# Performance work log

Hardware: AMD Instinct MI355X
Metric: run time of the kernel (lower is better)

The kernel has to match this reference:

```python
import jax, jax.numpy as jnp
import numpy as np

N = 20000      # num_sr == num_tg entities
D = 256        # ent_dim
DR = 256       # rel_dim
RNUM = 1000    # number of relations
Q = 128        # SVD rank
H = 4          # n_head
L = 2          # layers
E_RAND = 640000  # random edges (avg degree 32); N self-loops appended
LEAK = 0.2
EPS_LN = 1e-5


def _l2norm(x):
    # F.normalize(x, dim=1, p=2)
    return x / jnp.maximum(jnp.linalg.norm(x, axis=1, keepdims=True), 1e-12)


def _gat(x, src, dst, W, a_s, a_d):
    """Multi-head GAT layer on an edge list; heads are averaged so out dim == in dim.
    x: [N,D], W: [H,D,D], a_s/a_d: [H,D]."""
    n = x.shape[0]
    h = jnp.einsum('nd,hde->nhe', x, W)                  # [N,H,D]
    es = jnp.einsum('nhe,he->nh', h, a_s)                # [N,H]
    ed = jnp.einsum('nhe,he->nh', h, a_d)                # [N,H]
    e = jax.nn.leaky_relu(es[src] + ed[dst], LEAK)       # [E,H]
    # segment softmax over incoming edges of each dst node
    m = jax.ops.segment_max(e, dst, num_segments=n)      # [N,H]
    ex = jnp.exp(e - m[dst])
    den = jax.ops.segment_sum(ex, dst, num_segments=n)   # [N,H]
    attn = ex / (den[dst] + 1e-16)                       # [E,H]
    out = jax.ops.segment_sum(attn[:, :, None] * h[src], dst, num_segments=n)  # [N,H,D]
    return jax.nn.elu(out).mean(axis=1)                  # head average -> [N,D]


def _mha(x, wq, bq, wk, bk, wv, bv, fc_w, fc_b, ln_g, ln_b):
    """Standard post-norm multi-head self-attention over the 'ranges' axis. x: [N,R,D]."""
    n, r, d = x.shape
    def split(y):  # [N,R,H*D] -> [N,H,R,D]
        return y.reshape(n, r, H, d).transpose(0, 2, 1, 3)
    q, k, v = split(x @ wq + bq), split(x @ wk + bk), split(x @ wv + bv)
    attn = jax.nn.softmax(jnp.einsum('nhqd,nhkd->nhqk', q, k) / jnp.sqrt(jnp.float32(d)), axis=-1)
    o = jnp.einsum('nhqk,nhkd->nhqd', attn, v).transpose(0, 2, 1, 3).reshape(n, r, H * d)
    o = o @ fc_w + fc_b + x                              # output proj + residual
    mu = o.mean(-1, keepdims=True)
    var = o.var(-1, keepdims=True)
    return (o - mu) / jnp.sqrt(var + EPS_LN) * ln_g + ln_b


def _rel_agg(adj_in, adj_out, rel):
    # sparse-dense mm + row-sum normalize + concat (direct=True branch)
    ri = (adj_in @ rel) / (adj_in.sum(-1, keepdims=True) + 1e-5)
    ro = (adj_out @ rel) / (adj_out.sum(-1, keepdims=True) + 1e-5)
    return jnp.concatenate([ri, ro], axis=-1)            # [N, 2*DR]


def _forward(ent_sr, ent_tg, rel_sr, rel_tg, alpha,
             u_mul_s_sr, vt_sr, u_mul_s_tg, vt_tg,
             rel_adj_sr_in, rel_adj_sr_out, rel_adj_tg_in, rel_adj_tg_out,
             gat_W, gat_a_src, gat_a_dst,
             wq, bq, wk, bk, wv, bv, fc_w, fc_b, ln_g, ln_b,
             edges_sr, edges_tg):
    # --- Relation Aggregator (direct=True, phase='eval': aug == aggregated) ---
    sr_rel = _rel_agg(rel_adj_sr_in, rel_adj_sr_out, rel_sr)
    tg_rel = _rel_agg(rel_adj_tg_in, rel_adj_tg_out, rel_tg)
    aug_sr_rel, aug_tg_rel = sr_rel, tg_rel

    # --- Global Structure Aggregator: SVD-based propagation ---
    e_sr, e_tg = ent_sr, ent_tg
    for _ in range(L):
        g_sr = u_mul_s_sr @ (vt_sr @ e_sr)               # [N,Q]@([Q,N]@[N,D])
        g_tg = u_mul_s_tg @ (vt_tg @ e_tg)
        e_sr = jax.nn.relu(alpha * g_sr + (1.0 - alpha) * e_sr)
        e_tg = jax.nn.relu(alpha * g_tg + (1.0 - alpha) * e_tg)
    aug_sr = e_sr + ent_sr
    aug_tg = e_tg + ent_tg

    # --- Attentive Neighbor Aggregator (res=True; eval => dropout = identity) ---
    x_sr, x_tg = ent_sr, ent_tg
    sr_list, tg_list = [x_sr], [x_tg]
    for l in range(L):
        x_sr = _l2norm(_gat(x_sr, edges_sr[0], edges_sr[1], gat_W[l], gat_a_src[l], gat_a_dst[l]))
        x_tg = _l2norm(_gat(x_tg, edges_tg[0], edges_tg[1], gat_W[l], gat_a_src[l], gat_a_dst[l]))
        sr_list.append(x_sr)
        tg_list.append(x_tg)

    # --- multi-range neighborhood fusion ---
    sr = _mha(jnp.stack(sr_list, axis=1), wq, bq, wk, bk, wv, bv, fc_w, fc_b, ln_g, ln_b).mean(axis=1)
    tg = _mha(jnp.stack(tg_list, axis=1), wq, bq, wk, bk, wv, bv, fc_w, fc_b, ln_g, ln_b).mean(axis=1)

    # --- final fusion: neighbors + relation semantics ---
    sr_out = jnp.concatenate([sr, sr_rel], axis=-1)
    tg_out = jnp.concatenate([tg, tg_rel], axis=-1)
    aug_sr_out = jnp.concatenate([aug_sr, aug_sr_rel], axis=-1)
    aug_tg_out = jnp.concatenate([aug_tg, aug_tg_rel], axis=-1)
    return (sr_out, tg_out, aug_sr_out, aug_tg_out)


def setup_inputs() -> dict:
    key = jax.random.key(0)
    ks = jax.random.split(key, 32)
    def nrm(k, shape, s):
        return jax.random.normal(k, shape, jnp.float32) * s
    def edges(k):
        e = jax.random.randint(k, (2, E_RAND), 0, N, dtype=jnp.int32)
        loops = jnp.arange(N, dtype=jnp.int32)
        return jnp.concatenate([e, jnp.stack([loops, loops])], axis=1)  # [2, E_RAND+N]
    inp = {
        'ent_sr': nrm(ks[0], (N, D), 0.1),
        'ent_tg': nrm(ks[1], (N, D), 0.1),
        'rel_sr': nrm(ks[2], (RNUM, DR), 0.1),
        'rel_tg': nrm(ks[3], (RNUM, DR), 0.1),
        'alpha': jnp.float32(0.5),
        'u_mul_s_sr': nrm(ks[4], (N, Q), 0.05),
        'vt_sr': nrm(ks[5], (Q, N), 0.05),
        'u_mul_s_tg': nrm(ks[6], (N, Q), 0.05),
        'vt_tg': nrm(ks[7], (Q, N), 0.05),
        'rel_adj_sr_in': jax.random.uniform(ks[8], (N, RNUM), jnp.float32),
        'rel_adj_sr_out': jax.random.uniform(ks[9], (N, RNUM), jnp.float32),
        'rel_adj_tg_in': jax.random.uniform(ks[10], (N, RNUM), jnp.float32),
        'rel_adj_tg_out': jax.random.uniform(ks[11], (N, RNUM), jnp.float32),
        'gat_W': nrm(ks[12], (L, H, D, D), 1.0 / np.sqrt(D)),
        'gat_a_src': nrm(ks[13], (L, H, D), 1.0 / np.sqrt(D)),
        'gat_a_dst': nrm(ks[14], (L, H, D), 1.0 / np.sqrt(D)),
        'wq': nrm(ks[15], (D, H * D), 1.0 / np.sqrt(D)),
        'bq': jnp.zeros((H * D,), jnp.float32),
        'wk': nrm(ks[16], (D, H * D), 1.0 / np.sqrt(D)),
        'bk': jnp.zeros((H * D,), jnp.float32),
        'wv': nrm(ks[17], (D, H * D), 1.0 / np.sqrt(D)),
        'bv': jnp.zeros((H * D,), jnp.float32),
        'fc_w': nrm(ks[18], (H * D, D), 1.0 / np.sqrt(H * D)),
        'fc_b': jnp.zeros((D,), jnp.float32),
        'ln_g': jnp.ones((D,), jnp.float32),
        'ln_b': jnp.zeros((D,), jnp.float32),
        'edges_sr': edges(ks[19]),
        'edges_tg': edges(ks[20]),
    }
    return inp


def reference(ent_sr, ent_tg, rel_sr, rel_tg, alpha,
              u_mul_s_sr, vt_sr, u_mul_s_tg, vt_tg,
              rel_adj_sr_in, rel_adj_sr_out, rel_adj_tg_in, rel_adj_tg_out,
              gat_W, gat_a_src, gat_a_dst,
              wq, bq, wk, bk, wv, bv, fc_w, fc_b, ln_g, ln_b,
              edges_sr, edges_tg):
    return _forward(ent_sr, ent_tg, rel_sr, rel_tg, alpha,
                    u_mul_s_sr, vt_sr, u_mul_s_tg, vt_tg,
                    rel_adj_sr_in, rel_adj_sr_out, rel_adj_tg_in, rel_adj_tg_out,
                    gat_W, gat_a_src, gat_a_dst,
                    wq, bq, wk, bk, wv, bv, fc_w, fc_b, ln_g, ln_b,
                    edges_sr, edges_tg)
```

## Files before the change

### kernel.cpp

```cpp
#include <hip/hip_runtime.h>
#include <stdint.h>

typedef unsigned short u16;
typedef __bf16 bf16x8 __attribute__((ext_vector_type(8)));
typedef float f32x4 __attribute__((ext_vector_type(4)));

#define DEV static __device__ __forceinline__

DEV float bf2f(u16 u) { unsigned v = ((unsigned)u) << 16; float f; __builtin_memcpy(&f, &v, 4); return f; }
DEV u16 f2bf(float f) {
  unsigned x; __builtin_memcpy(&x, &f, 4);
  x += 0x7FFFu + ((x >> 16) & 1u);
  return (u16)(x >> 16);
}
DEV float wred_sum(float v) { for (int m = 32; m; m >>= 1) v += __shfl_xor(v, m); return v; }
DEV float wred_max(float v) { for (int m = 32; m; m >>= 1) v = fmaxf(v, __shfl_xor(v, m)); return v; }
DEV void wred_max4(f32x4& v) {
  for (int m = 32; m; m >>= 1) {
#pragma unroll
    for (int i = 0; i < 4; ++i) v[i] = fmaxf(v[i], __shfl_xor(v[i], m));
  }
}
DEV void wred_sum4(f32x4& v) {
  for (int m = 32; m; m >>= 1) {
#pragma unroll
    for (int i = 0; i < 4; ++i) v[i] += __shfl_xor(v[i], m);
  }
}

enum { M_ATOMIC = 0, M_SCALE2, M_BLEND, M_BF16, M_BF16B, M_F32B, M_PART };

template <int MODE>
__global__ __launch_bounds__(256) void k_gemm(
    const u16* __restrict__ A, const u16* __restrict__ B,
    int M, int lda, int ldb, int Ksteps, int kper,
    void* __restrict__ C1v, float* __restrict__ C2, int ldc,
    const float* __restrict__ rowsum, const float* __restrict__ ein, int ldein,
    const float* __restrict__ alphap, const float* __restrict__ bias,
    long hA, long hB, long hC, int nsplit, long hE)
{
  __shared__ u16 As[4096], Bs[4096];
  const int tid = threadIdx.x, lane = tid & 63, wid = tid >> 6;
  const long m0 = (long)blockIdx.x * 128, n0 = (long)blockIdx.y * 128;
  int ks, kend;
  long chead = 0;
  int hz = 0;
  if (hA | hB | hC) {
    int z = blockIdx.z;
    hz = z / nsplit;
    int sp = z - hz * nsplit;
    A += (long)hz * hA;
    B += (long)hz * hB;
    chead = (MODE == M_PART) ? (long)z * hC : (long)hz * hC;
    ks = sp * kper;
    kend = ks + kper; if (kend > Ksteps) kend = Ksteps;
  } else {
    ks = blockIdx.z * kper;
    kend = ks + kper; if (kend > Ksteps) kend = Ksteps;
  }
  if (MODE == M_BLEND) ein += (long)hz * hE;

  const u16 *ag[2], *bg[2];
  u16 *al[2], *bl[2];
#pragma unroll
  for (int i = 0; i < 2; ++i) {
    int s = (wid * 2 + i) * 64 + lane;
    int row = s >> 2, cs = (s & 3) ^ ((row >> 1) & 3);
    ag[i] = A + (m0 + row) * (long)lda + cs * 8;
    bg[i] = B + (n0 + row) * (long)ldb + cs * 8;
    al[i] = As + (wid * 2 + i) * 512;
    bl[i] = Bs + (wid * 2 + i) * 512;
  }
  const int kq = lane >> 4, rr = lane & 15;
  const int wm = wid >> 1, wn = wid & 1;

  f32x4 acc[4][4] = {};

  for (; ks < kend; ++ks) {
    long ko = (long)ks * 32;
#pragma unroll
    for (int i = 0; i < 2; ++i) {
      __builtin_amdgcn_global_load_lds((const __attribute__((address_space(1))) unsigned int*)(ag[i] + ko),
                                       (__attribute__((address_space(3))) unsigned int*)al[i], 16, 0, 0);
      __builtin_amdgcn_global_load_lds((const __attribute__((address_space(1))) unsigned int*)(bg[i] + ko),
                                       (__attribute__((address_space(3))) unsigned int*)bl[i], 16, 0, 0);
    }
    __syncthreads();
    bf16x8 af[4], bff[4];
#pragma unroll
    for (int i = 0; i < 4; ++i) {
      int ra = wm * 64 + i * 16 + rr, ca = kq ^ ((ra >> 1) & 3);
      af[i] = *(const bf16x8*)(As + ra * 32 + ca * 8);
      int rb = wn * 64 + i * 16 + rr, cb = kq ^ ((rb >> 1) & 3);
      bff[i] = *(const bf16x8*)(Bs + rb * 32 + cb * 8);
    }
#pragma unroll
    for (int i = 0; i < 4; ++i)
#pragma unroll
      for (int j = 0; j < 4; ++j)
        acc[i][j] = __builtin_amdgcn_mfma_f32_16x16x32_bf16(af[i], bff[j], acc[i][j], 0, 0, 0);
    __syncthreads();
  }

  float* Cf = (float*)C1v;
  u16* Cu = (u16*)C1v;
  const int r4 = (lane >> 4) << 2;
#pragma unroll
  for (int i = 0; i < 4; ++i) {
#pragma unroll
    for (int rg = 0; rg < 4; ++rg) {
      long row = m0 + wm * 64 + i * 16 + r4 + rg;
      if (row >= M) continue;
      float scale = 0.f, al_ = 0.f, ml_ = 0.f;
      if (MODE == M_SCALE2) scale = 1.f / (rowsum[(long)hz * M + row] + 1e-5f);
      if (MODE == M_BLEND) { al_ = *alphap; ml_ = 1.f - al_; }
#pragma unroll
      for (int j = 0; j < 4; ++j) {
        long col = n0 + wn * 64 + j * 16 + rr;
        float v = acc[i][j][rg];
        long idx = chead + row * (long)ldc + col;
        if (MODE == M_ATOMIC) atomicAdd(Cf + idx, v);
        else if (MODE == M_PART) Cf[idx] = v;
        else if (MODE == M_SCALE2) { float sv = v * scale; Cf[idx] = sv; C2[idx] = sv; }
        else if (MODE == M_BLEND) { float e = ein[row * (long)ldein + col]; Cf[idx] = fmaxf(al_ * v + ml_ * e, 0.f); }
        else if (MODE == M_BF16) Cu[idx] = f2bf(v);
        else if (MODE == M_BF16B) Cu[idx] = f2bf(v + bias[col]);
        else if (MODE == M_F32B) Cf[idx] = v + bias[col];
      }
    }
  }
}

__global__ void k_cvt(const float* __restrict__ in, u16* __restrict__ out, long R, long C, long Cp, long ostride)
{
  long idx = (long)blockIdx.x * blockDim.x + threadIdx.x;
  long cw = Cp >> 3;
  if (idx >= R * cw) return;
  long r = idx / cw, c8 = (idx % cw) << 3;
  u16 tmp[8];
  if (c8 < C) {
    const f32x4* p = (const f32x4*)(in + r * C + c8);
    f32x4 a = p[0], b = p[1];
#pragma unroll
    for (int i = 0; i < 4; ++i) { tmp[i] = f2bf(a[i]); tmp[4 + i] = f2bf(b[i]); }
  } else {
#pragma unroll
    for (int i = 0; i < 8; ++i) tmp[i] = 0;
  }
  uint4 w_; __builtin_memcpy(&w_, tmp, 16);
  *(uint4*)(out + r * ostride + c8) = w_;
}

__global__ __launch_bounds__(256) void k_cvtT(const float* __restrict__ in, u16* __restrict__ out,
                                              int Bh, int R, int C, int Rp)
{
  __shared__ float tile[64][65];
  int bid = blockIdx.x;
  int nrt = Rp >> 6;
  int rt = bid % nrt; bid /= nrt;
  int nct = C >> 6;
  int ct = bid % nct; int b = bid / nct;
  int t = threadIdx.x;
  int tr = t >> 4, tc4 = (t & 15) << 2;
#pragma unroll
  for (int i = 0; i < 4; ++i) {
    int r = (rt << 6) + tr + i * 16;
    f32x4 v = {0.f, 0.f, 0.f, 0.f};
    if (r < R) v = *(const f32x4*)(in + ((long)b * R + r) * C + (ct << 6) + tc4);
    tile[tr + i * 16][tc4 + 0] = v[0];
    tile[tr + i * 16][tc4 + 1] = v[1];
    tile[tr + i * 16][tc4 + 2] = v[2];
    tile[tr + i * 16][tc4 + 3] = v[3];
  }
  __syncthreads();
  int wc = t >> 4, wr4 = (t & 15) << 2;
#pragma unroll
  for (int i = 0; i < 4; ++i) {
    int c = wc + i * 16;
    u16 o[4];
#pragma unroll
    for (int k2 = 0; k2 < 4; ++k2) o[k2] = f2bf(tile[wr4 + k2][c]);
    unsigned long long pk; __builtin_memcpy(&pk, o, 8);
    *(unsigned long long*)(out + ((long)b * C + (ct << 6) + c) * Rp + (rt << 6) + wr4) = pk;
  }
}

__global__ __launch_bounds__(256) void k_adj4(const float* __restrict__ a0, const float* __restrict__ a1,
                                              const float* __restrict__ a2, const float* __restrict__ a3,
                                              u16* __restrict__ o01, u16* __restrict__ o23,
                                              float* __restrict__ rowsum, int C, int Cp, int N)
{
  int r = blockIdx.x, pl = blockIdx.y, t = threadIdx.x;
  const float* in = pl == 0 ? a0 : pl == 1 ? a1 : pl == 2 ? a2 : a3;
  u16* out = pl < 2 ? o01 + (size_t)pl * N * Cp : o23 + (size_t)(pl - 2) * N * Cp;
  f32x4 v = {0.f, 0.f, 0.f, 0.f};
  int c = t << 2;
  if (c + 3 < C) v = *(const f32x4*)(in + (long)r * C + c);
  u16 o[4];
#pragma unroll
  for (int i = 0; i < 4; ++i) o[i] = f2bf(v[i]);
  unsigned long long pk; __builtin_memcpy(&pk, o, 8);
  *(unsigned long long*)(out + (long)r * Cp + c) = pk;
  float s = wred_sum(v[0] + v[1] + v[2] + v[3]);
  __shared__ float ws4[4];
  if ((t & 63) == 0) ws4[t >> 6] = s;
  __syncthreads();
  if (t == 0) rowsum[(long)pl * N + r] = ws4[0] + ws4[1] + ws4[2] + ws4[3];
}

__global__ void k_red(const float* __restrict__ P, float* __restrict__ o, int NS)
{
  int i = blockIdx.x * 256 + threadIdx.x;
  int h = i >> 15, rem = i & 32767;
  const float* p = P + (long)h * NS * 32768 + rem;
  float s = 0.f;
  for (int k = 0; k < NS; ++k) s += p[(long)k * 32768];
  o[i] = s;
}

__global__ void k_zero_i(int* p, int n) { for (int i = blockIdx.x * blockDim.x + threadIdx.x; i < n; i += gridDim.x * blockDim.x) p[i] = 0; }
__global__ void k_copy_i(const int* __restrict__ a, int* __restrict__ b, int n) { for (int i = blockIdx.x * blockDim.x + threadIdx.x; i < n; i += gridDim.x * blockDim.x) b[i] = a[i]; }
__global__ void k_hist(const int* __restrict__ dst, int* __restrict__ deg, int E)
{ for (int i = blockIdx.x * blockDim.x + threadIdx.x; i < E; i += gridDim.x * blockDim.x) atomicAdd(&deg[dst[i]], 1); }
__global__ void k_scatter(const int* __restrict__ src, const int* __restrict__ dst, int* __restrict__ cur,
                          int* __restrict__ srcs, int E)
{
  for (int i = blockIdx.x * blockDim.x + threadIdx.x; i < E; i += gridDim.x * blockDim.x) {
    int p = atomicAdd(&cur[dst[i]], 1);
    srcs[p] = src[i];
  }
}
__global__ __launch_bounds__(1024) void k_scan(const int* __restrict__ deg, int* __restrict__ off, int n)
{
  __shared__ int bsum[1024];
  int t = threadIdx.x;
  int per = (n + 1023) >> 10;
  int s0 = t * per, s1 = s0 + per; if (s1 > n) s1 = n;
  int s = 0;
  for (int i = s0; i < s1; ++i) s += deg[i];
  bsum[t] = s;
  __syncthreads();
  for (int d = 1; d < 1024; d <<= 1) {
    int x = (t >= d) ? bsum[t - d] : 0;
    __syncthreads();
    bsum[t] += x;
    __syncthreads();
  }
  if (t == 0) off[0] = 0;
  int run = t ? bsum[t - 1] : 0;
  for (int i = s0; i < s1; ++i) { run += deg[i]; off[i + 1] = run; }
}

__global__ __launch_bounds__(256) void k_esed(const u16* __restrict__ h, const float* __restrict__ as_,
                                              const float* __restrict__ ad_, float* __restrict__ esq,
                                              float* __restrict__ ed, signed char* __restrict__ q8, int N)
{
  int n = blockIdx.x, t = threadIdx.x, hd = t >> 6, l = t & 63;
  long base = (long)n * 1024 + hd * 256 + (l << 2);
  ushort4 hv = *(const ushort4*)(h + base);
  float h0 = bf2f(hv.x), h1 = bf2f(hv.y), h2 = bf2f(hv.z), h3 = bf2f(hv.w);
  const float* ap = as_ + hd * 256 + (l << 2);
  const float* dp = ad_ + hd * 256 + (l << 2);
  float ps = h0 * ap[0] + h1 * ap[1] + h2 * ap[2] + h3 * ap[3];
  float pd = h0 * dp[0] + h1 * dp[1] + h2 * dp[2] + h3 * dp[3];
  ps = wred_sum(ps); pd = wred_sum(pd);
  float amax = fmaxf(fmaxf(fabsf(h0), fabsf(h1)), fmaxf(fabsf(h2), fabsf(h3)));
  amax = wred_max(amax);
  float rsc = amax > 0.f ? 127.f / amax : 0.f;
  signed char qb[4];
  qb[0] = (signed char)__float2int_rn(h0 * rsc);
  qb[1] = (signed char)__float2int_rn(h1 * rsc);
  qb[2] = (signed char)__float2int_rn(h2 * rsc);
  qb[3] = (signed char)__float2int_rn(h3 * rsc);
  int qw; __builtin_memcpy(&qw, qb, 4);
  *(int*)(q8 + base) = qw;
  if (l == 0) {
    esq[n * 8 + hd] = ps;
    esq[n * 8 + 4 + hd] = amax * (1.f / 127.f);
    ed[n * 4 + hd] = pd;
  }
}

__global__ __launch_bounds__(256) void k_gat(const signed char* __restrict__ q8,
                                             const float* __restrict__ esq, const float* __restrict__ ed,
                                             const int* __restrict__ off0, const int* __restrict__ srcs0,
                                             const int* __restrict__ off1, const int* __restrict__ srcs1,
                                             u16* __restrict__ x0, u16* __restrict__ x1, int N, int NPq)
{
  int t = threadIdx.x, w = t >> 6, l = t & 63;
  int n = blockIdx.x * 4 + w;
  if (n >= N) return;
  int side = blockIdx.y;
  const int* off = side ? off1 : off0;
  const int* srcs = side ? srcs1 : srcs0;
  u16* xout = side ? x1 : x0;
  size_t ofs = side ? (size_t)NPq : 0;
  q8 += ofs * 1024; esq += ofs * 8;

  int e0 = off[n], deg = off[n + 1] - e0;
  f32x4 edv = *(const f32x4*)(ed + (ofs + n) * 4);

  f32x4 m = {-1e30f, -1e30f, -1e30f, -1e30f};
  f32x4 psum = {0.f, 0.f, 0.f, 0.f};
  f32x4 acc0 = {0.f, 0.f, 0.f, 0.f};
  f32x4 acc1 = {0.f, 0.f, 0.f, 0.f};
  f32x4 acc2 = {0.f, 0.f, 0.f, 0.f};
  f32x4 acc3 = {0.f, 0.f, 0.f, 0.f};
  const long loff = l << 2;

  for (int base = 0; base < deg; base += 64) {
    int cnt = min(64, deg - base);
    bool act = l < cnt;
    int s = 0;
    f32x4 v = {-1e30f, -1e30f, -1e30f, -1e30f};
    if (act) {
      s = srcs[e0 + base + l];
      f32x4 es4 = *(const f32x4*)(esq + (long)s * 8);
#pragma unroll
      for (int hd = 0; hd < 4; ++hd) {
        float x = es4[hd] + edv[hd];
        v[hd] = x >= 0.f ? x : 0.2f * x;
      }
    }
    f32x4 mc = v;
    wred_max4(mc);
    f32x4 nm;
#pragma unroll
    for (int hd = 0; hd < 4; ++hd) nm[hd] = fmaxf(m[hd], mc[hd]);
    f32x4 sc;
#pragma unroll
    for (int hd = 0; hd < 4; ++hd) sc[hd] = __expf(m[hd] - nm[hd]);
    psum *= sc;
    acc0 *= sc[0]; acc1 *= sc[1]; acc2 *= sc[2]; acc3 *= sc[3];
    m = nm;
    f32x4 wq4 = {0.f, 0.f, 0.f, 0.f};
    if (act) {
      f32x4 qs4 = *(const f32x4*)(esq + (long)s * 8 + 4);
#pragma unroll
      for (int hd = 0; hd < 4; ++hd) {
        float e = __expf(v[hd] - m[hd]);
        psum[hd] += e;
        wq4[hd] = e * qs4[hd];
      }
    }
#pragma unroll 2
    for (int j = 0; j < cnt; ++j) {
      int sj = __shfl(s, j);
      float w0 = __shfl(wq4[0], j);
      float w1 = __shfl(wq4[1], j);
      float w2 = __shfl(wq4[2], j);
      float w3 = __shfl(wq4[3], j);
      const signed char* p = q8 + (long)sj * 1024 + loff;
      char4 c0 = *(const char4*)(p);
      char4 c1 = *(const char4*)(p + 256);
      char4 c2 = *(const char4*)(p + 512);
      char4 c3 = *(const char4*)(p + 768);
      acc0[0] += w0 * (float)c0.x; acc0[1] += w0 * (float)c0.y; acc0[2] += w0 * (float)c0.z; acc0[3] += w0 * (float)c0.w;
      acc1[0] += w1 * (float)c1.x; acc1[1] += w1 * (float)c1.y; acc1[2] += w1 * (float)c1.z; acc1[3] += w1 * (float)c1.w;
      acc2[0] += w2 * (float)c2.x; acc2[1] += w2 * (float)c2.y; acc2[2] += w2 * (float)c2.z; acc2[3] += w2 * (float)c2.w;
      acc3[0] += w3 * (float)c3.x; acc3[1] += w3 * (float)c3.y; acc3[2] += w3 * (float)c3.z; acc3[3] += w3 * (float)c3.w;
    }
  }
  wred_sum4(psum);
  f32x4 rd;
#pragma unroll
  for (int hd = 0; hd < 4; ++hd) rd[hd] = 1.f / (psum[hd] + 1e-16f);
  float mean[4]; float nrm = 0.f;
#pragma unroll
  for (int i = 0; i < 4; ++i) {
    float y0 = acc0[i] * rd[0]; y0 = y0 > 0.f ? y0 : __expf(y0) - 1.f;
    float y1 = acc1[i] * rd[1]; y1 = y1 > 0.f ? y1 : __expf(y1) - 1.f;
    float y2 = acc2[i] * rd[2]; y2 = y2 > 0.f ? y2 : __expf(y2) - 1.f;
    float y3 = acc3[i] * rd[3]; y3 = y3 > 0.f ? y3 : __expf(y3) - 1.f;
    float mv = 0.25f * (y0 + y1 + y2 + y3);
    mean[i] = mv; nrm += mv * mv;
  }
  nrm = wred_sum(nrm);
  float scn = 1.f / fmaxf(sqrtf(nrm), 1e-12f);
  u16 o[4];
#pragma unroll
  for (int i = 0; i < 4; ++i) o[i] = f2bf(mean[i] * scn);
  unsigned long long pk; __builtin_memcpy(&pk, o, 8);
  *(unsigned long long*)(xout + (long)n * 768 + loff) = pk;
}

__global__ void k_bias2(const float* __restrict__ wq, const float* __restrict__ wk,
                        const float* __restrict__ fcw,
                        const float* __restrict__ bq, const float* __restrict__ bk,
                        const float* __restrict__ bv,
                        float* __restrict__ vq1, float* __restrict__ vq2,
                        float* __restrict__ beff2, float* __restrict__ s3)
{
  int t = blockIdx.x * 256 + threadIdx.x;
  int h = t >> 8, d = t & 255;
  float a1 = 0.f, a2 = 0.f, a3 = 0.f;
  for (int j = 0; j < 256; ++j) {
    a1 += wk[(long)d * 1024 + h * 256 + j] * bq[h * 256 + j];
    a2 += wq[(long)d * 1024 + h * 256 + j] * bk[h * 256 + j];
    a3 += bv[h * 256 + j] * fcw[(long)(h * 256 + j) * 256 + d];
  }
  vq1[t] = a1; vq2[t] = a2; beff2[t] = a3;
  if (d == 0) {
    float s = 0.f;
    for (int j = 0; j < 256; ++j) s += bq[h * 256 + j] * bk[h * 256 + j];
    s3[h] = s;
  }
}

__global__ __launch_bounds__(256) void k_score2(const u16* __restrict__ x, const u16* __restrict__ kg,
                                                const float* __restrict__ vq1, const float* __restrict__ vq2,
                                                const float* __restrict__ s3, float* __restrict__ attn,
                                                int N, int NPq)
{
  int n = blockIdx.x, side = blockIdx.y, t = threadIdx.x, hd = t >> 6, l = t & 63;
  long rbase = (long)side * 3 * NPq + (long)n * 3;
  int i4 = l << 2;
  f32x4 xr[3], kc[3];
#pragma unroll
  for (int r = 0; r < 3; ++r) {
    ushort4 a = *(const ushort4*)(x + (rbase + r) * 256 + i4);
    xr[r][0] = bf2f(a.x); xr[r][1] = bf2f(a.y); xr[r][2] = bf2f(a.z); xr[r][3] = bf2f(a.w);
    ushort4 b = *(const ushort4*)(kg + (rbase + r) * 1024 + hd * 256 + i4);
    kc[r][0] = bf2f(b.x); kc[r][1] = bf2f(b.y); kc[r][2] = bf2f(b.z); kc[r][3] = bf2f(b.w);
  }
  f32x4 v1 = *(const f32x4*)(vq1 + hd * 256 + i4);
  f32x4 v2 = *(const f32x4*)(vq2 + hd * 256 + i4);
  float red[15];
#pragma unroll
  for (int r = 0; r < 3; ++r)
#pragma unroll
    for (int c = 0; c < 3; ++c) {
      f32x4 p = xr[r] * kc[c];
      red[r * 3 + c] = p[0] + p[1] + p[2] + p[3];
    }
#pragma unroll
  for (int c = 0; c < 3; ++c) {
    f32x4 p1 = xr[c] * v1;
    f32x4 p2 = xr[c] * v2;
    red[9 + c] = p1[0] + p1[1] + p1[2] + p1[3];
    red[12 + c] = p2[0] + p2[1] + p2[2] + p2[3];
  }
#pragma unroll
  for (int i = 0; i < 15; ++i) red[i] = wred_sum(red[i]);
  if (l == 0) {
    float s3h = s3[hd];
    float* out = attn + ((long)side * N + n) * 36 + hd * 9;
#pragma unroll
    for (int r = 0; r < 3; ++r) {
      float v0 = (red[r * 3 + 0] + red[9 + 0] + red[12 + r] + s3h) * 0.0625f;
      float v1_ = (red[r * 3 + 1] + red[9 + 1] + red[12 + r] + s3h) * 0.0625f;
      float v2_ = (red[r * 3 + 2] + red[9 + 2] + red[12 + r] + s3h) * 0.0625f;
      float mm = fmaxf(v0, fmaxf(v1_, v2_));
      float e0 = __expf(v0 - mm), e1 = __expf(v1_ - mm), e2 = __expf(v2_ - mm);
      float rs = 1.f / (e0 + e1 + e2);
      out[r * 3 + 0] = e0 * rs; out[r * 3 + 1] = e1 * rs; out[r * 3 + 2] = e2 * rs;
    }
  }
}

__global__ __launch_bounds__(256) void k_cln(const u16* __restrict__ vf, const float* __restrict__ attn,
                                             const u16* __restrict__ x, const float* __restrict__ fcb,
                                             const float* __restrict__ g, const float* __restrict__ b,
                                             float* __restrict__ out0, float* __restrict__ out1,
                                             int N, int NPq)
{
  int n = blockIdx.x, side = blockIdx.y, t = threadIdx.x, w = t >> 6, l = t & 63;
  long rbase = (long)side * 3 * NPq + (long)n * 3;
  float* out = (side ? out1 : out0) + (long)n * 768;
  __shared__ float aa[36];
  __shared__ float ybuf[3][256];
  if (t < 36) aa[t] = attn[((long)side * N + n) * 36 + t];
  __syncthreads();
  if (w < 3) {
    int d4 = l << 2;
    f32x4 acc = {0.f, 0.f, 0.f, 0.f};
#pragma unroll
    for (int h = 0; h < 4; ++h)
#pragma unroll
      for (int rp = 0; rp < 3; ++rp) {
        float wgt = aa[h * 9 + w * 3 + rp];
        ushort4 vv = *(const ushort4*)(vf + (rbase + rp) * 1024 + h * 256 + d4);
        acc[0] += wgt * bf2f(vv.x); acc[1] += wgt * bf2f(vv.y);
        acc[2] += wgt * bf2f(vv.z); acc[3] += wgt * bf2f(vv.w);
      }
    f32x4 fb = *(const f32x4*)(fcb + d4);
    ushort4 xu = *(const ushort4*)(x + (rbase + w) * 256 + d4);
    acc[0] += fb[0] + bf2f(xu.x); acc[1] += fb[1] + bf2f(xu.y);
    acc[2] += fb[2] + bf2f(xu.z); acc[3] += fb[3] + bf2f(xu.w);
    float s1 = acc[0] + acc[1] + acc[2] + acc[3];
    float s2 = acc[0] * acc[0] + acc[1] * acc[1] + acc[2] * acc[2] + acc[3] * acc[3];
    s1 = wred_sum(s1); s2 = wred_sum(s2);
    float mu = s1 * 0.00390625f;
    float var = s2 * 0.00390625f - mu * mu;
    float rs = rsqrtf(var + 1e-5f);
#pragma unroll
    for (int i = 0; i < 4; ++i) {
      int d = d4 + i;
      ybuf[w][d] = (acc[i] - mu) * rs * g[d] + b[d];
    }
  }
  __syncthreads();
  if (t < 64) {
#pragma unroll
    for (int i = 0; i < 4; ++i) {
      int d = (t << 2) + i;
      out[d] = (ybuf[0][d] + ybuf[1][d] + ybuf[2][d]) * (1.f / 3.f);
    }
  }
}

__global__ void k_aug(const float* __restrict__ e, const float* __restrict__ ent0,
                      const float* __restrict__ ent1, float* __restrict__ out, int N)
{
  long i = (long)blockIdx.x * blockDim.x + threadIdx.x;
  if (i >= (long)N * 128) return;
  int side = i >= (long)N * 64;
  long ii = side ? i - (long)N * 64 : i;
  const float* ent = side ? ent1 : ent0;
  long n = ii >> 6; int d4 = (int)(ii & 63) << 2;
  f32x4 a = *(const f32x4*)(e + ((long)side * N + n) * 256 + d4);
  f32x4 c = *(const f32x4*)(ent + n * 256 + d4);
  *(f32x4*)(out + ((long)side * N + n) * 768 + d4) = a + c;
}

extern "C" void kernel_launch(void* const* d_in, const int* in_sizes, int n_in,
                              void* d_out, int out_size, void* d_ws, size_t ws_size,
                              hipStream_t stream)
{
  (void)n_in; (void)out_size; (void)ws_size;
  const int N = 20000, NP = 20096, RNUM = 1000, RP = 1024;
  const int NT2 = NP + N;
  const int NS = 64;
  const int Es = in_sizes[26] / 2, Et = in_sizes[27] / 2;

  const float* ent_sr = (const float*)d_in[0];
  const float* ent_tg = (const float*)d_in[1];
  const float* rel_in[2] = {(const float*)d_in[2], (const float*)d_in[3]};
  const float* alphap = (const float*)d_in[4];
  const float* ums[2] = {(const float*)d_in[5], (const float*)d_in[7]};
  const float* vt[2]  = {(const float*)d_in[6], (const float*)d_in[8]};
  const float* adj[4] = {(const float*)d_in[9], (const float*)d_in[10], (const float*)d_in[11], (const float*)d_in[12]};
  const float* gat_W  = (const float*)d_in[13];
  const float* gat_as = (const float*)d_in[14];
  const float* gat_ad = (const float*)d_in[15];
  const float* wq = (const float*)d_in[16]; const float* bq = (const float*)d_in[17];
  const float* wk = (const float*)d_in[18]; const float* bk = (const float*)d_in[19];
  const float* wv = (const float*)d_in[20]; const float* bv = (const float*)d_in[21];
  const float* fcw = (const float*)d_in[22]; const float* fcb = (const float*)d_in[23];
  const float* lng = (const float*)d_in[24]; const float* lnb = (const float*)d_in[25];
  const int* edges[2] = {(const int*)d_in[26], (const int*)d_in[27]};
  const int Ecnt[2] = {Es, Et};

  float* out0 = (float*)d_out;
  float* out1 = out0 + (size_t)N * 768;
  float* out2 = out1 + (size_t)N * 768;
  float* out3 = out2 + (size_t)N * 768;

  char* wsp = (char*)d_ws; size_t wo = 0;
  auto alloc = [&](size_t bytes) { void* p = wsp + wo; wo = (wo + bytes + 255) & ~(size_t)255; return p; };

  u16* A_sr = (u16*)alloc((size_t)NP * 768 * 2);
  u16* A_tg = (u16*)alloc((size_t)NP * 768 * 2);
  u16* QBUF = (u16*)alloc((size_t)3 * NT2 * 1024 * 2);
  u16* KBUF = (u16*)alloc((size_t)3 * NT2 * 1024 * 2);
  float* PART = (float*)alloc((size_t)2 * NS * 32768 * 4);
  float* rowsum = (float*)alloc((size_t)4 * N * 4);
  u16* relT[2] = {(u16*)alloc(256 * RP * 2), (u16*)alloc(256 * RP * 2)};
  u16* WtG = (u16*)alloc((size_t)2 * 1024 * 256 * 2);
  u16* fcT = (u16*)alloc(256 * 1024 * 2);
  u16* wqB = (u16*)alloc(256 * 1024 * 2);
  u16* wkB = (u16*)alloc(256 * 1024 * 2);
  u16* wvB = (u16*)alloc(256 * 1024 * 2);
  u16* gT  = (u16*)alloc((size_t)4 * 256 * 256 * 2);
  u16* vfT = (u16*)alloc((size_t)4 * 256 * 256 * 2);
  float* vq1 = (float*)alloc(1024 * 4);
  float* vq2 = (float*)alloc(1024 * 4);
  float* beff2 = (float*)alloc(1024 * 4);
  float* s3b = (float*)alloc(4 * 4);
  float* esqb = (float*)alloc((size_t)NT2 * 8 * 4);
  float* edb = (float*)alloc((size_t)NT2 * 4 * 4);
  float* attn = (float*)alloc((size_t)2 * N * 36 * 4);
  int* off_[2]; int* cur_[2]; int* srcs_[2];
  for (int s = 0; s < 2; ++s) {
    off_[s] = (int*)alloc((size_t)(N + 4) * 4);
    cur_[s] = (int*)alloc((size_t)(N + 4) * 4);
    srcs_[s] = (int*)alloc((size_t)Ecnt[s] * 4);
  }
  float* tT2 = (float*)alloc((size_t)2 * 256 * 128 * 4);
  u16* tTb2 = (u16*)alloc((size_t)2 * 256 * 128 * 2);

  u16* hbuf = QBUF;
  u16* vfbuf = QBUF;
  u16* adjbQ = QBUF;
  u16* adjbK = KBUF;
  float* e_b = (float*)KBUF;
  u16* eT = (u16*)(e_b + (size_t)2 * N * 256);
  u16* vtb0 = eT + (size_t)2 * 256 * NP;
  u16* umb0 = vtb0 + (size_t)2 * 128 * NP;
  signed char* q8buf = (signed char*)KBUF;
  u16* kgbuf = KBUF;

  const float* ent_s[2] = {ent_sr, ent_tg};

  auto cvt = [&](const float* in, u16* out, long R, long C, long Cp, long ostr) {
    long total = R * (Cp >> 3);
    int blocks = (int)((total + 255) / 256);
    k_cvt<<<blocks, 256, 0, stream>>>(in, out, R, C, Cp, ostr);
  };
  auto cvtT = [&](const float* in, u16* out, int Bh, int R, int C, int Rp) {
    int blocks = (Rp >> 6) * (C >> 6) * Bh;
    k_cvtT<<<blocks, 256, 0, stream>>>(in, out, Bh, R, C, Rp);
  };
  auto gemm = [&](int mode, const u16* A, const u16* B, int M, int lda, int ldb, int Kp, int Nt,
                  int zdim, int nsplit,
                  void* C1, float* C2, int ldc, const float* rs, const float* ein, int ldein,
                  const float* alp, const float* bias,
                  long hA = 0, long hB = 0, long hC = 0, long hE = 0) {
    int Ks = Kp >> 5;
    bool hmode = (hA | hB | hC) != 0;
    int kper = hmode ? (Ks + nsplit - 1) / nsplit
                     : (zdim > 1 ? (Ks + zdim - 1) / zdim : Ks);
    dim3 g((M + 127) >> 7, Nt, zdim);
    switch (mode) {
      case M_ATOMIC: k_gemm<M_ATOMIC><<<g, 256, 0, stream>>>(A, B, M, lda, ldb, Ks, kper, C1, C2, ldc, rs, ein, ldein, alp, bias, hA, hB, hC, nsplit, hE); break;
      case M_SCALE2: k_gemm<M_SCALE2><<<g, 256, 0, stream>>>(A, B, M, lda, ldb, Ks, kper, C1, C2, ldc, rs, ein, ldein, alp, bias, hA, hB, hC, nsplit, hE); break;
      case M_BLEND:  k_gemm<M_BLEND><<<g, 256, 0, stream>>>(A, B, M, lda, ldb, Ks, kper, C1, C2, ldc, rs, ein, ldein, alp, bias, hA, hB, hC, nsplit, hE); break;
      case M_BF16:   k_gemm<M_BF16><<<g, 256, 0, stream>>>(A, B, M, lda, ldb, Ks, kper, C1, C2, ldc, rs, ein, ldein, alp, bias, hA, hB, hC, nsplit, hE); break;
      case M_BF16B:  k_gemm<M_BF16B><<<g, 256, 0, stream>>>(A, B, M, lda, ldb, Ks, kper, C1, C2, ldc, rs, ein, ldein, alp, bias, hA, hB, hC, nsplit, hE); break;
      case M_F32B:   k_gemm<M_F32B><<<g, 256, 0, stream>>>(A, B, M, lda, ldb, Ks, kper, C1, C2, ldc, rs, ein, ldein, alp, bias, hA, hB, hC, nsplit, hE); break;
      case M_PART:   k_gemm<M_PART><<<g, 256, 0, stream>>>(A, B, M, lda, ldb, Ks, kper, C1, C2, ldc, rs, ein, ldein, alp, bias, hA, hB, hC, nsplit, hE); break;
    }
  };

  for (int s = 0; s < 2; ++s) {
    k_zero_i<<<80, 256, 0, stream>>>(cur_[s], N);
    k_hist<<<1024, 256, 0, stream>>>(edges[s] + Ecnt[s], cur_[s], Ecnt[s]);
    k_scan<<<1, 1024, 0, stream>>>(cur_[s], off_[s], N);
    k_copy_i<<<80, 256, 0, stream>>>(off_[s], cur_[s], N);
    k_scatter<<<1024, 256, 0, stream>>>(edges[s], edges[s] + Ecnt[s], cur_[s], srcs_[s], Ecnt[s]);
  }

  cvtT(rel_in[0], relT[0], 1, RNUM, 256, RP);
  cvtT(rel_in[1], relT[1], 1, RNUM, 256, RP);
  {
    dim3 ga(N, 4);
    k_adj4<<<ga, 256, 0, stream>>>(adj[0], adj[1], adj[2], adj[3], adjbQ, adjbK, rowsum, RNUM, RP, N);
  }
  gemm(M_SCALE2, adjbQ, relT[0], N, RP, RP, RP, 2, 2, 1,
       out0 + 256, out2 + 256, 768, rowsum, nullptr, 0, nullptr, nullptr,
       (long)N * RP, 0, 256);
  gemm(M_SCALE2, adjbK, relT[1], N, RP, RP, RP, 2, 2, 1,
       out1 + 256, out3 + 256, 768, rowsum + 2 * N, nullptr, 0, nullptr, nullptr,
       (long)N * RP, 0, 256);

  cvt(vt[0], vtb0, 128, N, NP, NP);
  cvt(vt[1], vtb0 + (size_t)128 * NP, 128, N, NP, NP);
  cvt(ums[0], umb0, N, 128, 128, 128);
  cvt(ums[1], umb0 + (size_t)NP * 128, N, 128, 128, 128);
  for (int l = 0; l < 2; ++l) {
    if (l == 0) {
      cvtT(ent_sr, eT, 1, N, 256, NP);
      cvtT(ent_tg, eT + (size_t)256 * NP, 1, N, 256, NP);
    } else {
      cvtT(e_b, eT, 2, N, 256, NP);
    }
    gemm(M_PART, eT, vtb0, 256, NP, NP, NP, 1, 2 * NS, NS,
         PART, nullptr, 128, nullptr, nullptr, 0, nullptr, nullptr,
         (long)256 * NP, (long)128 * NP, 32768);
    k_red<<<256, 256, 0, stream>>>(PART, tT2, NS);
    cvt(tT2, tTb2, 512, 128, 128, 128);
    if (l == 0) {
      for (int s = 0; s < 2; ++s)
        gemm(M_BLEND, umb0 + (size_t)s * NP * 128, tTb2 + (size_t)s * 32768, N, 128, 128, 128, 2, 1, 1,
             e_b + (size_t)s * N * 256, nullptr, 256, nullptr, ent_s[s], 256, alphap, nullptr);
    } else {
      gemm(M_BLEND, umb0, tTb2, N, 128, 128, 128, 2, 2, 1,
           e_b, nullptr, 256, nullptr, e_b, 256, alphap, nullptr,
           (long)NP * 128, 32768, (long)N * 256, (long)N * 256);
    }
  }
  k_aug<<<(int)(((long)N * 128 + 255) / 256), 256, 0, stream>>>(e_b, ent_sr, ent_tg, out2, N);

  cvt(ent_sr, A_sr, N, 256, 256, 768);
  cvt(ent_tg, A_tg, N, 256, 256, 768);
  cvtT(gat_W, WtG, 8, 256, 256, 256);
  for (int l = 0; l < 2; ++l) {
    gemm(M_BF16, A_sr + l * 256, WtG + (size_t)l * 1024 * 256, NT2, 768, 256, 256, 8, 1, 1,
         hbuf, nullptr, 1024, nullptr, nullptr, 0, nullptr, nullptr);
    k_esed<<<NT2, 256, 0, stream>>>(hbuf, gat_as + l * 1024, gat_ad + l * 1024, esqb, edb, q8buf, NT2);
    dim3 gg((N + 3) / 4, 2);
    k_gat<<<gg, 256, 0, stream>>>(q8buf, esqb, edb, off_[0], srcs_[0], off_[1], srcs_[1],
                                  A_sr + (l + 1) * 256, A_tg + (l + 1) * 256, N, NP);
  }

  cvt(wq, wqB, 256, 1024, 1024, 1024);
  cvt(wk, wkB, 256, 1024, 1024, 1024);
  cvt(wv, wvB, 256, 1024, 1024, 1024);
  cvtT(fcw, fcT, 1, 1024, 256, 1024);
  k_bias2<<<4, 256, 0, stream>>>(wq, wk, fcw, bq, bk, bv, vq1, vq2, beff2, s3b);
  gemm(M_BF16, wqB, wkB, 256, 1024, 1024, 256, 2, 4, 1, gT, nullptr, 256,
       nullptr, nullptr, 0, nullptr, nullptr, 256, 256, 65536);
  gemm(M_BF16, fcT, wvB, 256, 1024, 1024, 256, 2, 4, 1, vfT, nullptr, 256,
       nullptr, nullptr, 0, nullptr, nullptr, 256, 256, 65536);

  gemm(M_BF16, A_sr, gT, 3 * NT2, 256, 256, 256, 8, 1, 1, kgbuf, nullptr, 1024,
       nullptr, nullptr, 0, nullptr, nullptr);
  {
    dim3 gs(N, 2);
    k_score2<<<gs, 256, 0, stream>>>(A_sr, kgbuf, vq1, vq2, s3b, attn, N, NP);
  }
  gemm(M_BF16B, A_sr, vfT, 3 * NT2, 256, 256, 256, 8, 1, 1, vfbuf, nullptr, 1024,
       nullptr, nullptr, 0, nullptr, beff2);
  {
    dim3 gc(N, 2);
    k_cln<<<gc, 256, 0, stream>>>(vfbuf, attn, A_sr, fcb, lng, lnb, out0, out1, N, NP);
  }
}
```

Before: 1.732 ms.

## Interleave int8 head features per lane and broadcast edge weights via LDS

The int8 quantized features are rewritten in an interleaved layout, so each lane's 4 elements from all 4 heads sit in one 16-byte chunk. The GAT gather can then fetch a neighbour row with a single uint4 load per lane instead of four char4 loads. Per-edge source indices and weights are broadcast through shared memory instead of five shuffles per edge, and the unroll factor is raised. The cost is an extra block sync and LDS staging in the quantize kernel, and more LDS traffic in the gather loop. Because the gather kernel only writes its per-wave LDS slots before reading them, this relies on wave-level execution for ordering.

```diff
diff --git a/kernel.cpp b/kernel.cpp
--- a/kernel.cpp
+++ b/kernel.cpp
@@ -255,6 +255,7 @@
                                               const float* __restrict__ ad_, float* __restrict__ esq,
                                               float* __restrict__ ed, signed char* __restrict__ q8, int N)
 {
+  __shared__ int stg[4][64];
   int n = blockIdx.x, t = threadIdx.x, hd = t >> 6, l = t & 63;
   long base = (long)n * 1024 + hd * 256 + (l << 2);
   ushort4 hv = *(const ushort4*)(h + base);
@@ -273,11 +274,24 @@
   qb[2] = (signed char)__float2int_rn(h2 * rsc);
   qb[3] = (signed char)__float2int_rn(h3 * rsc);
   int qw; __builtin_memcpy(&qw, qb, 4);
-  *(int*)(q8 + base) = qw;
+  stg[hd][l] = qw;
   if (l == 0) {
     esq[n * 8 + hd] = ps;
     esq[n * 8 + 4 + hd] = amax * (1.f / 127.f);
     ed[n * 4 + hd] = pd;
+  }
+  __syncthreads();
+  if (t < 64) {
+    int b0 = stg[0][t], b1 = stg[1][t], b2 = stg[2][t], b3 = stg[3][t];
+    unsigned r[4];
+#pragma unroll
+    for (int i = 0; i < 4; ++i) {
+      int sh = 8 * i;
+      r[i] = ((unsigned)((b0 >> sh) & 0xff)) | ((unsigned)((b1 >> sh) & 0xff) << 8) |
+             ((unsigned)((b2 >> sh) & 0xff) << 16) | ((unsigned)((b3 >> sh) & 0xff) << 24);
+    }
+    uint4 o; __builtin_memcpy(&o, r, 16);
+    *(uint4*)(q8 + (long)n * 1024 + (t << 4)) = o;
   }
 }
 
@@ -287,6 +301,8 @@
                                              const int* __restrict__ off1, const int* __restrict__ srcs1,
                                              u16* __restrict__ x0, u16* __restrict__ x1, int N, int NPq)
 {
+  __shared__ f32x4 sw[4][64];
+  __shared__ int ss[4][64];
   int t = threadIdx.x, w = t >> 6, l = t & 63;
   int n = blockIdx.x * 4 + w;
   if (n >= N) return;
@@ -343,22 +359,22 @@
         wq4[hd] = e * qs4[hd];
       }
     }
-#pragma unroll 2
+    sw[w][l] = wq4;
+    ss[w][l] = s;
+#pragma unroll 4
     for (int j = 0; j < cnt; ++j) {
-      int sj = __shfl(s, j);
-      float w0 = __shfl(wq4[0], j);
-      float w1 = __shfl(wq4[1], j);
-      float w2 = __shfl(wq4[2], j);
-      float w3 = __shfl(wq4[3], j);
-      const signed char* p = q8 + (long)sj * 1024 + loff;
-      char4 c0 = *(const char4*)(p);
-      char4 c1 = *(const char4*)(p + 256);
-      char4 c2 = *(const char4*)(p + 512);
-      char4 c3 = *(const char4*)(p + 768);
-      acc0[0] += w0 * (float)c0.x; acc0[1] += w0 * (float)c0.y; acc0[2] += w0 * (float)c0.z; acc0[3] += w0 * (float)c0.w;
-      acc1[0] += w1 * (float)c1.x; acc1[1] += w1 * (float)c1.y; acc1[2] += w1 * (float)c1.z; acc1[3] += w1 * (float)c1.w;
-      acc2[0] += w2 * (float)c2.x; acc2[1] += w2 * (float)c2.y; acc2[2] += w2 * (float)c2.z; acc2[3] += w2 * (float)c2.w;
-      acc3[0] += w3 * (float)c3.x; acc3[1] += w3 * (float)c3.y; acc3[2] += w3 * (float)c3.z; acc3[3] += w3 * (float)c3.w;
+      f32x4 w4 = sw[w][j];
+      int sj = ss[w][j];
+      uint4 c = *(const uint4*)(q8 + (long)sj * 1024 + (l << 4));
+      const int* cw = (const int*)&c;
+#pragma unroll
+      for (int i = 0; i < 4; ++i) {
+        int ci = cw[i];
+        acc0[i] += w4[0] * (float)((signed char)(ci));
+        acc1[i] += w4[1] * (float)((signed char)(ci >> 8));
+        acc2[i] += w4[2] * (float)((signed char)(ci >> 16));
+        acc3[i] += w4[3] * (float)(ci >> 24);
+      }
     }
   }
   wred_sum4(psum);
```

After: 1.711 ms. Within noise of the previous version (-1.3%).
